# Performance work log

Measured on AMD Instinct MI355X. Metric: run time of the kernel, lower is better.

Reference implementation:

```python
import jax, jax.numpy as jnp
import numpy as np

# norse default parameters
DT = 1e-3
TAU_MEM_INV = 100.0      # 1/1e-2
TAU_SYN_INV = 200.0      # 1/5e-3
TAU_ADAPT_INV = 1.0 / 700.0
V_TH = 1.0
BETA = 1.8
ALPHA = 100.0            # SuperSpike surrogate slope
T = 40                   # encoder seq length
SCALE = 50.0

@jax.custom_vjp
def spike(x):
    return (x > 0).astype(x.dtype)

def _spike_fwd(x):
    return (x > 0).astype(x.dtype), x

def _spike_bwd(x, g):
    # SuperSpike surrogate gradient
    return (g / (ALPHA * jnp.abs(x) + 1.0) ** 2,)

spike.defvjp(_spike_fwd, _spike_bwd)

def encode(c):
    # LIF constant-current encoder: c (B, D) -> spikes (T, B, D)
    def step(v, _):
        v = v + DT * TAU_MEM_INV * (c - v)
        z = spike(v - V_TH)
        return v * (1.0 - z), z
    _, zs = jax.lax.scan(step, jnp.zeros_like(c), None, length=T)
    return zs

def _forward(x, w_in, w_rec, w_out):
    B = x.shape[0]
    H = w_in.shape[0]
    O = w_out.shape[0]
    x_pos = encode(jax.nn.relu(SCALE * x))
    x_neg = encode(jax.nn.relu(-SCALE * x))
    xs = jnp.concatenate([x_pos, x_neg], axis=2)  # (T, B, 2*D)

    z0 = jnp.zeros((B, H), x.dtype)
    v0 = jnp.zeros((B, H), x.dtype)
    i0 = jnp.zeros((B, H), x.dtype)
    b0 = jnp.full((B, H), V_TH, x.dtype)  # adaptive threshold starts at v_th
    vo0 = jnp.zeros((B, O), x.dtype)
    io0 = jnp.zeros((B, O), x.dtype)

    def step(carry, x_t):
        z, v, i, b, vo, io = carry
        # LSNN cell (norse lsnn_step)
        v_dec = v + DT * TAU_MEM_INV * (0.0 - v + i)
        i_dec = i - DT * TAU_SYN_INV * i
        b_dec = b + DT * TAU_ADAPT_INV * (V_TH - b)
        z_new = spike(v_dec - b_dec)
        v_new = (1.0 - z_new) * v_dec  # v_reset = 0
        i_new = i_dec + x_t @ w_in.T + z @ w_rec.T
        b_new = b_dec + z_new * (TAU_ADAPT_INV * BETA)
        # LI readout (norse li_step); dropout is identity in eval mode
        vo_new = vo + DT * TAU_MEM_INV * (0.0 - vo + io)
        io_new = io - DT * TAU_SYN_INV * io + z_new @ w_out.T
        return (z_new, v_new, i_new, b_new, vo_new, io_new), vo_new

    _, voltages = jax.lax.scan(step, (z0, v0, i0, b0, vo0, io0), xs)  # (T, B, O)
    m = jnp.max(voltages, axis=0)
    return jax.nn.softmax(m, axis=1)

def setup_inputs():
    key = jax.random.key(0)
    k1, k2, k3, k4 = jax.random.split(key, 4)
    B, D, H, O = 16384, 4, 128, 2
    return {
        "x": jax.random.normal(k1, (B, D), jnp.float32),
        "w_in": jax.random.normal(k2, (H, 2 * D), jnp.float32) / np.sqrt(2 * D).astype(np.float32),
        "w_rec": jax.random.normal(k3, (H, H), jnp.float32) / np.sqrt(H).astype(np.float32),
        "w_out": jax.random.normal(k4, (O, H), jnp.float32) / np.sqrt(H).astype(np.float32),
    }

def reference(x, w_in, w_rec, w_out):
    return _forward(x, w_in, w_rec, w_out)
```

## Files before the change

kernel.cpp:

```cpp
#include <hip/hip_runtime.h>
#include <stdint.h>

#define HID 128
#define BPB 16

__device__ __forceinline__ void wave_reduce_add2(float& a, float& b) {
  asm("v_add_f32 %0, %0, %0 row_shr:1 bound_ctrl:0\n\t"
      "v_add_f32 %1, %1, %1 row_shr:1 bound_ctrl:0\n\t"
      "v_add_f32 %0, %0, %0 row_shr:2 bound_ctrl:0\n\t"
      "v_add_f32 %1, %1, %1 row_shr:2 bound_ctrl:0\n\t"
      "v_add_f32 %0, %0, %0 row_shr:4 bound_ctrl:0\n\t"
      "v_add_f32 %1, %1, %1 row_shr:4 bound_ctrl:0\n\t"
      "v_add_f32 %0, %0, %0 row_shr:8 bound_ctrl:0\n\t"
      "v_add_f32 %1, %1, %1 row_shr:8 bound_ctrl:0\n\t"
      "v_add_f32 %0, %0, %0 row_bcast:15 row_mask:0xa\n\t"
      "v_add_f32 %1, %1, %1 row_bcast:15 row_mask:0xa\n\t"
      "v_add_f32 %0, %0, %0 row_bcast:31 row_mask:0xc\n\t"
      "v_add_f32 %1, %1, %1 row_bcast:31 row_mask:0xc\n\t"
      : "+v"(a), "+v"(b));
}

__global__ __launch_bounds__(1024, 4) void lsnn_fwd(
    const float* __restrict__ x,
    const float* __restrict__ w_in,
    const float* __restrict__ w_rec,
    const float* __restrict__ w_out,
    float* __restrict__ out,
    int B)
{
#pragma clang fp contract(off)
  __shared__ float2 wt[HID * 64];

  const int tid = threadIdx.x;
#pragma unroll
  for (int m = 0; m < 8; ++m) {
    int idx = m * 1024 + tid;
    int k = idx & 127;
    int l = idx >> 7;
    float a = w_rec[l * HID + k];
    float c = w_rec[(l + 64) * HID + k];
    wt[(k << 6) | (l ^ (k & 63))] = make_float2(a, c);
  }
  __syncthreads();

  const int lane = tid & 63;
  const int b = blockIdx.x * BPB + (tid >> 6);
  if (b >= B) return;

  const int j0 = lane;
  const int j1 = lane + 64;

  float cc[4], ev[4];
  float wsel0[4], wsel1[4];
  {
#pragma unroll
    for (int c = 0; c < 4; ++c) {
      float p = 50.0f * x[b * 4 + c];
      cc[c] = fabsf(p);
      ev[c] = 0.0f;
      int col = (p > 0.0f) ? c : (c + 4);
      wsel0[c] = w_in[j0 * 8 + col];
      wsel1[c] = w_in[j1 * 8 + col];
    }
  }

  uint64_t pk[5];
#pragma unroll
  for (int tw = 0; tw < 5; ++tw) {
    uint64_t pw = 0;
    for (int ts = 0; ts < 8; ++ts) {
      unsigned byte = 0;
#pragma unroll
      for (int c = 0; c < 4; ++c) {
        ev[c] = ev[c] + 0.1f * (cc[c] - ev[c]);
        if (ev[c] - 1.0f > 0.0f) {
          byte |= (1u << c);
          ev[c] = 0.0f;
        }
      }
      pw |= ((uint64_t)byte) << (ts << 3);
    }
    pk[tw] = pw;
  }

  const float wo00 = w_out[j0], wo01 = w_out[j1];
  const float wo10 = w_out[HID + j0], wo11 = w_out[HID + j1];

  float v0 = 0.f, v1 = 0.f, i0 = 0.f, i1 = 0.f, b0 = 1.0f, b1 = 1.0f;
  float io0 = 0.f, io1 = 0.f, vo0 = 0.f, vo1 = 0.f;
  float mm0 = -INFINITY, mm1 = -INFINITY;
  uint64_t zm0 = 0ull, zm1 = 0ull;

  const char* wtb = (const char*)wt;
  const int vb = lane << 3;

#pragma unroll
  for (int tw = 0; tw < 5; ++tw) {
    uint64_t pw = pk[tw];
    for (int ts = 0; ts < 8; ++ts) {
      float vd0 = v0 + 0.1f * (i0 - v0);
      float vd1 = v1 + 0.1f * (i1 - v1);
      float id0 = i0 - 0.2f * i0;
      float id1 = i1 - 0.2f * i1;
      float bd0 = b0 + 1.4285714285714286e-06f * (1.0f - b0);
      float bd1 = b1 + 1.4285714285714286e-06f * (1.0f - b1);
      bool z0 = (vd0 - bd0) > 0.0f;
      bool z1 = (vd1 - bd1) > 0.0f;
      v0 = z0 ? 0.0f : vd0;
      v1 = z1 ? 0.0f : vd1;
      b0 = bd0 + (z0 ? 0.0025714285714285714f : 0.0f);
      b1 = bd1 + (z1 ? 0.0025714285714285714f : 0.0f);

      float p0 = (z0 ? wo00 : 0.0f) + (z1 ? wo01 : 0.0f);
      float p1 = (z0 ? wo10 : 0.0f) + (z1 ? wo11 : 0.0f);
      wave_reduce_add2(p0, p1);

      float von0 = vo0 + 0.1f * (io0 - vo0);
      float von1 = vo1 + 0.1f * (io1 - vo1);
      io0 = (io0 - 0.2f * io0) + p0;
      io1 = (io1 - 0.2f * io1) + p1;
      vo0 = von0;
      vo1 = von1;
      mm0 = fmaxf(mm0, von0);
      mm1 = fmaxf(mm1, von1);

      int xb = (int)((pw >> (ts << 3)) & 0xFF);
      float ai0 = 0.f, ai1 = 0.f;
#pragma unroll
      for (int c = 0; c < 4; ++c) {
        if (xb & (1 << c)) {
          ai0 += wsel0[c];
          ai1 += wsel1[c];
        }
      }

      float ar0 = 0.f, ar1 = 0.f;
      uint64_t m0 = zm0;
      while (m0) {
        int k = __builtin_ctzll(m0);
        m0 &= m0 - 1;
        int soff = k * 520;
        float2 w = *(const float2*)(wtb + (vb ^ soff));
        ar0 += w.x;
        ar1 += w.y;
      }
      uint64_t m1 = zm1;
      while (m1) {
        int k = __builtin_ctzll(m1);
        m1 &= m1 - 1;
        int soff = 32768 + k * 520;
        float2 w = *(const float2*)(wtb + (vb ^ soff));
        ar0 += w.x;
        ar1 += w.y;
      }

      i0 = (id0 + ai0) + ar0;
      i1 = (id1 + ai1) + ar1;

      zm0 = __ballot(z0);
      zm1 = __ballot(z1);
    }
  }

  if (lane == 63) {
    float mx = fmaxf(mm0, mm1);
    float e0 = expf(mm0 - mx);
    float e1 = expf(mm1 - mx);
    float s = e0 + e1;
    out[b * 2 + 0] = e0 / s;
    out[b * 2 + 1] = e1 / s;
  }
}

extern "C" void kernel_launch(void* const* d_in, const int* in_sizes, int n_in,
                              void* d_out, int out_size, void* d_ws, size_t ws_size,
                              hipStream_t stream) {
  (void)n_in; (void)out_size; (void)d_ws; (void)ws_size;
  const float* x = (const float*)d_in[0];
  const float* w_in = (const float*)d_in[1];
  const float* w_rec = (const float*)d_in[2];
  const float* w_out = (const float*)d_in[3];
  float* out = (float*)d_out;
  int B = in_sizes[0] / 4;
  int blocks = (B + BPB - 1) / BPB;
  lsnn_fwd<<<blocks, 1024, 0, stream>>>(x, w_in, w_rec, w_out, out, B);
}
```

Baseline: 146.6 us.

## Vectorize LSNN state with packed float2 math and simplify recurrent weight LDS layout

Switches the paired per-lane neuron state and updates to two-wide float vectors so the compiler can emit packed FP32 instructions (v_pk_add/mul). Drops the XOR-swizzled shared-memory layout for the transposed recurrent weights in favour of a plain layout with shift-based addressing, and splits the 64-bit spike-mask walks into four 32-bit loops. It also issues the spike ballot earlier and makes the input-spike byte wave-uniform with readfirstlane. The aim is fewer VALU instructions per timestep and cheaper address arithmetic in the sparse recurrent accumulation, at some risk of LDS bank behaviour changing without the swizzle.

```diff
diff --git a/kernel.cpp b/kernel.cpp
--- a/kernel.cpp
+++ b/kernel.cpp
@@ -3,6 +3,8 @@
 
 #define HID 128
 #define BPB 16
+
+typedef float v2f __attribute__((ext_vector_type(2)));
 
 __device__ __forceinline__ void wave_reduce_add2(float& a, float& b) {
   asm("v_add_f32 %0, %0, %0 row_shr:1 bound_ctrl:0\n\t"
@@ -35,11 +37,9 @@
 #pragma unroll
   for (int m = 0; m < 8; ++m) {
     int idx = m * 1024 + tid;
-    int k = idx & 127;
-    int l = idx >> 7;
-    float a = w_rec[l * HID + k];
-    float c = w_rec[(l + 64) * HID + k];
-    wt[(k << 6) | (l ^ (k & 63))] = make_float2(a, c);
+    int l = idx & 63;
+    int k = idx >> 6;
+    wt[(k << 6) | l] = make_float2(w_rec[l * HID + k], w_rec[(l + 64) * HID + k]);
   }
   __syncthreads();
 
@@ -49,9 +49,10 @@
 
   const int j0 = lane;
   const int j1 = lane + 64;
+  const v2f zero2 = {0.0f, 0.0f};
 
   float cc[4], ev[4];
-  float wsel0[4], wsel1[4];
+  v2f wsel[4];
   {
 #pragma unroll
     for (int c = 0; c < 4; ++c) {
@@ -59,8 +60,8 @@
       cc[c] = fabsf(p);
       ev[c] = 0.0f;
       int col = (p > 0.0f) ? c : (c + 4);
-      wsel0[c] = w_in[j0 * 8 + col];
-      wsel1[c] = w_in[j1 * 8 + col];
+      wsel[c].x = w_in[j0 * 8 + col];
+      wsel[c].y = w_in[j1 * 8 + col];
     }
   }
 
@@ -83,12 +84,13 @@
     pk[tw] = pw;
   }
 
-  const float wo00 = w_out[j0], wo01 = w_out[j1];
-  const float wo10 = w_out[HID + j0], wo11 = w_out[HID + j1];
+  v2f wop0, wop1;
+  wop0.x = w_out[j0];       wop0.y = w_out[HID + j0];
+  wop1.x = w_out[j1];       wop1.y = w_out[HID + j1];
 
-  float v0 = 0.f, v1 = 0.f, i0 = 0.f, i1 = 0.f, b0 = 1.0f, b1 = 1.0f;
-  float io0 = 0.f, io1 = 0.f, vo0 = 0.f, vo1 = 0.f;
-  float mm0 = -INFINITY, mm1 = -INFINITY;
+  v2f vv = zero2, ii = zero2, io = zero2, vo = zero2;
+  v2f bb = {1.0f, 1.0f};
+  v2f mm = {-INFINITY, -INFINITY};
   uint64_t zm0 = 0ull, zm1 = 0ull;
 
   const char* wtb = (const char*)wt;
@@ -98,74 +100,72 @@
   for (int tw = 0; tw < 5; ++tw) {
     uint64_t pw = pk[tw];
     for (int ts = 0; ts < 8; ++ts) {
-      float vd0 = v0 + 0.1f * (i0 - v0);
-      float vd1 = v1 + 0.1f * (i1 - v1);
-      float id0 = i0 - 0.2f * i0;
-      float id1 = i1 - 0.2f * i1;
-      float bd0 = b0 + 1.4285714285714286e-06f * (1.0f - b0);
-      float bd1 = b1 + 1.4285714285714286e-06f * (1.0f - b1);
-      bool z0 = (vd0 - bd0) > 0.0f;
-      bool z1 = (vd1 - bd1) > 0.0f;
-      v0 = z0 ? 0.0f : vd0;
-      v1 = z1 ? 0.0f : vd1;
-      b0 = bd0 + (z0 ? 0.0025714285714285714f : 0.0f);
-      b1 = bd1 + (z1 ? 0.0025714285714285714f : 0.0f);
+      v2f vd = vv + 0.1f * (ii - vv);
+      v2f id = ii - 0.2f * ii;
+      v2f one_minus_b = {1.0f - bb.x, 1.0f - bb.y};
+      v2f bd = bb + 1.4285714285714286e-06f * one_minus_b;
+      bool z0 = (vd.x - bd.x) > 0.0f;
+      bool z1 = (vd.y - bd.y) > 0.0f;
+      uint64_t nz0 = __ballot(z0);
+      uint64_t nz1 = __ballot(z1);
+      vv.x = z0 ? 0.0f : vd.x;
+      vv.y = z1 ? 0.0f : vd.y;
+      bb.x = bd.x + (z0 ? 0.0025714285714285714f : 0.0f);
+      bb.y = bd.y + (z1 ? 0.0025714285714285714f : 0.0f);
 
-      float p0 = (z0 ? wo00 : 0.0f) + (z1 ? wo01 : 0.0f);
-      float p1 = (z0 ? wo10 : 0.0f) + (z1 ? wo11 : 0.0f);
+      v2f pp = (z0 ? wop0 : zero2) + (z1 ? wop1 : zero2);
+      float p0 = pp.x, p1 = pp.y;
       wave_reduce_add2(p0, p1);
 
-      float von0 = vo0 + 0.1f * (io0 - vo0);
-      float von1 = vo1 + 0.1f * (io1 - vo1);
-      io0 = (io0 - 0.2f * io0) + p0;
-      io1 = (io1 - 0.2f * io1) + p1;
-      vo0 = von0;
-      vo1 = von1;
-      mm0 = fmaxf(mm0, von0);
-      mm1 = fmaxf(mm1, von1);
+      v2f von = vo + 0.1f * (io - vo);
+      v2f pv; pv.x = p0; pv.y = p1;
+      io = (io - 0.2f * io) + pv;
+      vo = von;
+      mm.x = fmaxf(mm.x, von.x);
+      mm.y = fmaxf(mm.y, von.y);
 
-      int xb = (int)((pw >> (ts << 3)) & 0xFF);
-      float ai0 = 0.f, ai1 = 0.f;
-#pragma unroll
-      for (int c = 0; c < 4; ++c) {
-        if (xb & (1 << c)) {
-          ai0 += wsel0[c];
-          ai1 += wsel1[c];
+      int xb = __builtin_amdgcn_readfirstlane((int)((pw >> (ts << 3)) & 0xFF));
+      v2f ai = zero2;
+      if (xb & 1) ai += wsel[0];
+      if (xb & 2) ai += wsel[1];
+      if (xb & 4) ai += wsel[2];
+      if (xb & 8) ai += wsel[3];
+
+      v2f ar = zero2;
+      {
+        uint32_t m0 = (uint32_t)zm0;
+        while (m0) {
+          int k = __builtin_ctz(m0); m0 &= m0 - 1;
+          ar += *(const v2f*)(wtb + ((k << 9) | vb));
+        }
+        uint32_t m1 = (uint32_t)(zm0 >> 32);
+        while (m1) {
+          int k = __builtin_ctz(m1); m1 &= m1 - 1;
+          ar += *(const v2f*)(wtb + 16384 + ((k << 9) | vb));
+        }
+        uint32_t m2 = (uint32_t)zm1;
+        while (m2) {
+          int k = __builtin_ctz(m2); m2 &= m2 - 1;
+          ar += *(const v2f*)(wtb + 32768 + ((k << 9) | vb));
+        }
+        uint32_t m3 = (uint32_t)(zm1 >> 32);
+        while (m3) {
+          int k = __builtin_ctz(m3); m3 &= m3 - 1;
+          ar += *(const v2f*)(wtb + 49152 + ((k << 9) | vb));
         }
       }
 
-      float ar0 = 0.f, ar1 = 0.f;
-      uint64_t m0 = zm0;
-      while (m0) {
-        int k = __builtin_ctzll(m0);
-        m0 &= m0 - 1;
-        int soff = k * 520;
-        float2 w = *(const float2*)(wtb + (vb ^ soff));
-        ar0 += w.x;
-        ar1 += w.y;
-      }
-      uint64_t m1 = zm1;
-      while (m1) {
-        int k = __builtin_ctzll(m1);
-        m1 &= m1 - 1;
-        int soff = 32768 + k * 520;
-        float2 w = *(const float2*)(wtb + (vb ^ soff));
-        ar0 += w.x;
-        ar1 += w.y;
-      }
+      ii = (id + ai) + ar;
 
-      i0 = (id0 + ai0) + ar0;
-      i1 = (id1 + ai1) + ar1;
-
-      zm0 = __ballot(z0);
-      zm1 = __ballot(z1);
+      zm0 = nz0;
+      zm1 = nz1;
     }
   }
 
   if (lane == 63) {
-    float mx = fmaxf(mm0, mm1);
-    float e0 = expf(mm0 - mx);
-    float e1 = expf(mm1 - mx);
+    float mx = fmaxf(mm.x, mm.y);
+    float e0 = expf(mm.x - mx);
+    float e1 = expf(mm.y - mx);
     float s = e0 + e1;
     out[b * 2 + 0] = e0 / s;
     out[b * 2 + 1] = e1 / s;
```

Measured after the change: 150.9 us. 2.9% more time.
